# Kernel optimization log

Measured on AMD Instinct MI355X. Metric: run time of the kernel, lower is better.

The kernel has to match this reference:

```python
import jax, jax.numpy as jnp
import numpy as np

B, T, V, D, L, FFM = 2, 2048, 50257, 1024, 8, 2


def setup_inputs() -> dict:
    key = jax.random.key(0)
    ks = jax.random.split(key, 10)
    s = 0.02
    return {
        "input_ids": jax.random.randint(ks[0], (B, T), 0, V),
        "embed": jax.random.normal(ks[1], (V, D), jnp.float32) * s,
        "norm1_w": jnp.ones((L, D), jnp.float32),
        "norm2_w": jnp.ones((L, D), jnp.float32),
        "a_diag": jax.random.uniform(ks[2], (L, D), jnp.float32, 0.5, 0.99),
        "W_in": jax.random.normal(ks[3], (L, D, D), jnp.float32) * s,
        "b_in": jnp.zeros((L, D), jnp.float32),
        "W_out": jax.random.normal(ks[4], (L, D, D), jnp.float32) * s,
        "ff_w1": jax.random.normal(ks[5], (L, D, FFM * D), jnp.float32) * s,
        "ff_b1": jnp.zeros((L, FFM * D), jnp.float32),
        "ff_w2": jax.random.normal(ks[6], (L, FFM * D, D), jnp.float32) * s,
        "ff_b2": jnp.zeros((L, D), jnp.float32),
        "final_norm_w": jnp.ones((D,), jnp.float32),
        "lm_head_w": jax.random.normal(ks[7], (V, D), jnp.float32) * s,
    }


def rmsnorm(x, w, eps=1e-6):
    return x * jax.lax.rsqrt(jnp.mean(x * x, axis=-1, keepdims=True) + eps) * w


def chaos_core(x, a, Win, bin_, Wout):
    pre = jnp.einsum('btd,de->bte', x, Win) + bin_  # precompute input drive (parallel)

    def step(s, p):
        s = jnp.tanh(a * s + p)
        return s, s

    s0 = jnp.zeros((x.shape[0], x.shape[-1]), x.dtype)
    _, hs = jax.lax.scan(step, s0, jnp.swapaxes(pre, 0, 1))  # (T, B, D)
    hs = jnp.swapaxes(hs, 0, 1)  # (B, T, D)
    return jnp.einsum('btd,de->bte', hs, Wout)


def reference(input_ids, embed, norm1_w, norm2_w, a_diag, W_in, b_in, W_out,
              ff_w1, ff_b1, ff_w2, ff_b2, final_norm_w, lm_head_w):
    x = embed[input_ids]  # (B, T, D)
    for i in range(L):
        # input_norm -> core -> residual
        x = x + chaos_core(rmsnorm(x, norm1_w[i]), a_diag[i], W_in[i], b_in[i], W_out[i])
        # ff_norm -> FeedForward (Linear -> SiLU -> Linear) -> residual
        h = rmsnorm(x, norm2_w[i])
        h = jax.nn.silu(jnp.einsum('btd,df->btf', h, ff_w1[i]) + ff_b1[i])
        x = x + jnp.einsum('btf,fd->btd', h, ff_w2[i]) + ff_b2[i]
    x = rmsnorm(x, final_norm_w)
    return jnp.einsum('btd,vd->btv', x, lm_head_w)  # logits (B, T, V)
```

## Files before the change

### kernel.cpp

```cpp
#include <hip/hip_runtime.h>

typedef unsigned short u16;
typedef __bf16 bf16x8 __attribute__((ext_vector_type(8)));
typedef float f32x4 __attribute__((ext_vector_type(4)));
typedef unsigned short u16x4 __attribute__((ext_vector_type(4)));

__device__ __forceinline__ u16 f2bf(float f) {
  union { float f; unsigned int u; } v; v.f = f;
  return (u16)((v.u + 0x7FFFu + ((v.u >> 16) & 1u)) >> 16);
}

__device__ __forceinline__ void gload16(const void* g, void* l) {
  __builtin_amdgcn_global_load_lds(
      (const __attribute__((address_space(1))) unsigned int*)g,
      (__attribute__((address_space(3))) unsigned int*)l, 16, 0, 0);
}

__global__ void transpose_cast_kernel(const float* __restrict__ W, u16* __restrict__ WT,
                                      int R, int C) {
  __shared__ float tile[32][33];
  const int tx = threadIdx.x, ty = threadIdx.y;
  const size_t zoff = (size_t)blockIdx.z * R * C;
  const int c0 = blockIdx.x * 32, r0 = blockIdx.y * 32;
#pragma unroll
  for (int k = 0; k < 32; k += 8)
    tile[ty + k][tx] = W[zoff + (size_t)(r0 + ty + k) * C + (c0 + tx)];
  __syncthreads();
#pragma unroll
  for (int k = 0; k < 32; k += 8)
    WT[zoff + (size_t)(c0 + ty + k) * R + (r0 + tx)] = f2bf(tile[tx][ty + k]);
}

__global__ void lm_cast_kernel(const float* __restrict__ lm, u16* __restrict__ out) {
  const int row = blockIdx.x;
  const int t = threadIdx.x;
  u16x4 o = {0, 0, 0, 0};
  if (row < 50257) {
    float4 v = *(const float4*)(lm + (size_t)row * 1024 + t * 4);
    o.x = f2bf(v.x); o.y = f2bf(v.y); o.z = f2bf(v.z); o.w = f2bf(v.w);
  }
  *(u16x4*)(out + (size_t)row * 1024 + t * 4) = o;
}

__global__ void embed_kernel(const int* __restrict__ ids, const float* __restrict__ embed,
                             float* __restrict__ x) {
  const int row = blockIdx.x;
  const int id = ids[row];
  const int t = threadIdx.x;
  *(float4*)(x + (size_t)row * 1024 + t * 4) =
      *(const float4*)(embed + (size_t)id * 1024 + t * 4);
}

__global__ void rmsnorm_kernel(const float* __restrict__ x, const float* __restrict__ w,
                               u16* __restrict__ out) {
  const int row = blockIdx.x, tid = threadIdx.x;
  const float* xr = x + (size_t)row * 1024;
  float4 v = *(const float4*)(xr + tid * 4);
  float ss = v.x * v.x + v.y * v.y + v.z * v.z + v.w * v.w;
#pragma unroll
  for (int off = 32; off; off >>= 1) ss += __shfl_xor(ss, off);
  __shared__ float red[4];
  if ((tid & 63) == 0) red[tid >> 6] = ss;
  __syncthreads();
  const float tot = red[0] + red[1] + red[2] + red[3];
  const float r = rsqrtf(tot * (1.0f / 1024.0f) + 1e-6f);
  float4 wv = *(const float4*)(w + tid * 4);
  u16x4 o;
  o.x = f2bf(v.x * r * wv.x); o.y = f2bf(v.y * r * wv.y);
  o.z = f2bf(v.z * r * wv.z); o.w = f2bf(v.w * r * wv.w);
  *(u16x4*)(out + (size_t)row * 1024 + tid * 4) = o;
}

__device__ __forceinline__ void sload(const float* __restrict__ p, int tb,
                                      float A2b, float (&buf)[8]) {
#pragma unroll
  for (int j = 0; j < 8; j++)
    buf[j] = fmaf(p[(size_t)(tb + j) * 1024], 2.8853900817779268f, A2b);
}

__device__ __forceinline__ void scomp(float (&buf)[8], float m2A2, float& r,
                                      u16* __restrict__ o, int tb) {
#pragma unroll
  for (int j = 0; j < 8; j++) {
    float z = fmaf(m2A2, r, buf[j]);
    float e = __builtin_amdgcn_exp2f(z);
    r = __builtin_amdgcn_rcpf(1.0f + e);
    o[(size_t)(tb + j) * 1024] = f2bf(fmaf(-2.0f, r, 1.0f));
  }
}

__global__ __launch_bounds__(256) void scan_kernel(const float* __restrict__ pre,
                                                   const float* __restrict__ a_diag,
                                                   const float* __restrict__ b_in,
                                                   u16* __restrict__ hs) {
  const int T = 2048;
  const int idx = blockIdx.x * 256 + threadIdx.x;
  const int b = idx >> 10, d = idx & 1023;
  const float* p = pre + (size_t)b * T * 1024 + d;
  u16* o = hs + (size_t)b * T * 1024 + d;
  const float A2 = a_diag[d] * 2.8853900817779268f;
  const float A2b = fmaf(2.8853900817779268f, b_in[d], A2);
  const float m2A2 = -2.0f * A2;
  float r = 0.5f;
  float b0[8], b1[8], b2[8], b3[8];
  sload(p, 0, A2b, b0); sload(p, 8, A2b, b1);
  sload(p, 16, A2b, b2); sload(p, 24, A2b, b3);
  for (int t0 = 0; t0 < T; t0 += 32) {
    scomp(b0, m2A2, r, o, t0);
    if (t0 + 32 < T) sload(p, t0 + 32, A2b, b0);
    scomp(b1, m2A2, r, o, t0 + 8);
    if (t0 + 32 < T) sload(p, t0 + 40, A2b, b1);
    scomp(b2, m2A2, r, o, t0 + 16);
    if (t0 + 32 < T) sload(p, t0 + 48, A2b, b2);
    scomp(b3, m2A2, r, o, t0 + 24);
    if (t0 + 32 < T) sload(p, t0 + 56, A2b, b3);
  }
}

template <int EPI>
__global__ __launch_bounds__(256) void gemmL(
    const u16* __restrict__ A, int lda, const u16* __restrict__ Bw, int ldb,
    const float* __restrict__ bias, float* Cf, u16* __restrict__ Cb,
    int ldc, int K) {
  __shared__ char lds[49152];
  const int tid = threadIdx.x;
  const int lane = tid & 63;
  const int wc = tid >> 6;
  const int tm = blockIdx.y * 64, tn = blockIdx.x * 128;
  const int lr = lane & 15;
  const int sb0 = ((lane >> 4) ^ (lane & 7)) << 4;

  const int srow = tid >> 3;
  const int sxs = ((tid & 7) ^ (srow & 7)) << 4;
  const char* pA = (const char*)A + (size_t)(tm + srow) * lda * 2 + sxs;
  const char* pB = (const char*)Bw + (size_t)(tn + srow) * ldb * 2 + sxs;
  const size_t a32 = (size_t)lda * 64;
  const size_t b32 = (size_t)ldb * 64;

#define STGL(kt, bufo)                                \
  {                                                   \
    char* d = lds + (bufo) + tid * 16;                \
    const size_t kb = (size_t)(kt) << 7;              \
    gload16(pA + kb, d);                              \
    gload16(pA + a32 + kb, d + 4096);                 \
    gload16(pB + kb, d + 8192);                       \
    gload16(pB + b32 + kb, d + 12288);                \
    gload16(pB + 2 * b32 + kb, d + 16384);            \
    gload16(pB + 3 * b32 + kb, d + 20480);            \
  }

  f32x4 acc[4][2] = {};
  const int nkt = K >> 6;

  STGL(0, 0);
  int cur = 0;
  for (int kt = 0; kt < nkt; ++kt) {
    if (kt + 1 < nkt) {
      STGL(kt + 1, (cur ^ 1) * 24576);
      asm volatile("s_waitcnt vmcnt(6)" ::: "memory");
    } else {
      asm volatile("s_waitcnt vmcnt(0)" ::: "memory");
    }
    __builtin_amdgcn_s_barrier();
    const char* base = lds + cur * 24576;
    bf16x8 aF[4][2], bF[2][2];
#pragma unroll
    for (int m = 0; m < 4; m++)
#pragma unroll
      for (int ks = 0; ks < 2; ks++)
        aF[m][ks] =
            *(const bf16x8*)(base + (m * 16 + lr) * 128 + (sb0 ^ (ks << 6)));
#pragma unroll
    for (int n = 0; n < 2; n++)
#pragma unroll
      for (int ks = 0; ks < 2; ks++)
        bF[n][ks] = *(const bf16x8*)(base + 8192 +
                                     (wc * 32 + n * 16 + lr) * 128 +
                                     (sb0 ^ (ks << 6)));
#pragma unroll
    for (int ks = 0; ks < 2; ks++)
#pragma unroll
      for (int m = 0; m < 4; m++)
#pragma unroll
        for (int n = 0; n < 2; n++)
          acc[m][n] = __builtin_amdgcn_mfma_f32_16x16x32_bf16(
              aF[m][ks], bF[n][ks], acc[m][n], 0, 0, 0);
    __builtin_amdgcn_s_barrier();
    cur ^= 1;
  }
#undef STGL

  const int crow = tm + ((lane >> 4) << 2);
  const int ccol = tn + wc * 32 + lr;
#pragma unroll
  for (int m = 0; m < 4; m++) {
#pragma unroll
    for (int n = 0; n < 2; n++) {
      const int cg = ccol + n * 16;
      float bb = 0.0f;
      if (EPI == 2 || EPI == 3) bb = bias[cg];
#pragma unroll
      for (int j = 0; j < 4; j++) {
        const size_t off = (size_t)(crow + m * 16 + j) * ldc + cg;
        const float v = acc[m][n][j] + bb;
        if (EPI == 0) {
          Cf[off] = v;
        } else if (EPI == 1) {
          Cf[off] += v;
        } else if (EPI == 2) {
          const float sg = __builtin_amdgcn_rcpf(
              1.0f + __builtin_amdgcn_exp2f(-1.4426950408889634f * v));
          Cb[off] = f2bf(v * sg);
        } else {
          Cf[off] += v;
        }
      }
    }
  }
}

__global__ __launch_bounds__(512, 2) void gemm_lm8(
    const u16* __restrict__ A, const u16* __restrict__ Bw,
    float* __restrict__ C, int Nreal) {
  __shared__ char lds[131072];
  const int tid = threadIdx.x;
  const int lane = tid & 63;
  const int wid = tid >> 6;
  const int wr = wid >> 2;
  const int wc = wid & 3;
  const int bid = blockIdx.x;
  const int tm = (((bid & 7) << 1) + ((bid >> 3) & 1)) << 8;
  const int tn = (bid >> 4) << 8;

  const int srow = tid >> 3;
  const int sxor = ((tid & 7) ^ (srow & 7)) << 4;
  const char* pAs = (const char*)A + ((size_t)(tm + srow) << 11) + sxor;
  const char* pBs = (const char*)Bw + ((size_t)(tn + srow) << 11) + sxor;

#define STG(p, h, kt, ro)                                      \
  {                                                            \
    char* d = lds + (ro) + tid * 16;                           \
    const char* s = (p) + ((size_t)(h) << 18) + ((kt) << 7);   \
    gload16(s, d);                                             \
    gload16(s + (64ull << 11), d + 8192);                      \
  }

  const int lr = lane & 15;
  const int sb0 = (((lane >> 4) ^ (lane & 7)) << 4);
  const int sb[2] = {sb0, sb0 ^ 64};
  const int aB = wr * 16384 + lr * 128;
  const int bB = 32768 + (wc >> 1) * 16384 + ((wc & 1) * 64 + lr) * 128;

  bf16x8 aR[4][2], bR[2][2][2];
  f32x4 acc[8][4] = {};

#define LDA_Q(bufo, mq)                                                         \
  _Pragma("unroll") for (int m_ = 0; m_ < 4; m_++)                              \
  _Pragma("unroll") for (int k_ = 0; k_ < 2; k_++)                              \
      aR[m_][k_] = *(const bf16x8*)(lds + (bufo) + aB + (mq)*8192 + m_*2048 + sb[k_]);

#define LDB_Q(bufo, nq)                                                         \
  _Pragma("unroll") for (int n_ = 0; n_ < 2; n_++)                              \
  _Pragma("unroll") for (int k_ = 0; k_ < 2; k_++)                              \
      bR[nq][n_][k_] = *(const bf16x8*)(lds + (bufo) + bB + (nq)*4096 + n_*2048 + sb[k_]);

#define MFMA_Q(mq, nq)                                                          \
  __builtin_amdgcn_s_setprio(1);                                                \
  _Pragma("unroll") for (int m_ = 0; m_ < 4; m_++)                              \
  _Pragma("unroll") for (int n_ = 0; n_ < 2; n_++)                              \
  _Pragma("unroll") for (int k_ = 0; k_ < 2; k_++)                              \
      acc[(mq)*4 + m_][(nq)*2 + n_] = __builtin_amdgcn_mfma_f32_16x16x32_bf16(  \
          aR[m_][k_], bR[nq][n_][k_], acc[(mq)*4 + m_][(nq)*2 + n_], 0, 0, 0);  \
  __builtin_amdgcn_s_setprio(0);

#define BAR() __builtin_amdgcn_s_barrier()
#define LGKM0() asm volatile("s_waitcnt lgkmcnt(0)" ::: "memory")

  STG(pAs, 0, 0, 0);
  STG(pAs, 1, 0, 16384);
  STG(pBs, 0, 0, 32768);
  STG(pBs, 1, 0, 49152);
  STG(pBs, 0, 1, 65536 + 32768);
  STG(pBs, 1, 1, 65536 + 49152);
  asm volatile("s_waitcnt vmcnt(4)" ::: "memory");
  BAR();

  for (int it = 0; it < 8; ++it) {
    const int t1 = 2 * it + 1, t2 = 2 * it + 2, t3 = 2 * it + 3;
    const bool st = (it < 7);
    LDA_Q(0, 0); LDB_Q(0, 0);
    STG(pAs, 0, t1, 65536);
    BAR(); LGKM0(); MFMA_Q(0, 0); BAR();
    LDB_Q(0, 1);
    STG(pAs, 1, t1, 65536 + 16384);
    BAR(); LGKM0(); MFMA_Q(0, 1); BAR();
    LDA_Q(0, 1);
    if (st) STG(pBs, 0, t2, 32768);
    BAR(); LGKM0(); MFMA_Q(1, 0); BAR();
    if (st) STG(pBs, 1, t2, 49152);
    BAR(); LGKM0(); MFMA_Q(1, 1);
    if (st) { asm volatile("s_waitcnt vmcnt(4)" ::: "memory"); }
    else    { asm volatile("s_waitcnt vmcnt(0)" ::: "memory"); }
    BAR();
    LDA_Q(65536, 0); LDB_Q(65536, 0);
    if (st) STG(pAs, 0, t2, 0);
    BAR(); LGKM0(); MFMA_Q(0, 0); BAR();
    LDB_Q(65536, 1);
    if (st) STG(pAs, 1, t2, 16384);
    BAR(); LGKM0(); MFMA_Q(0, 1); BAR();
    LDA_Q(65536, 1);
    if (st) STG(pBs, 0, t3, 65536 + 32768);
    BAR(); LGKM0(); MFMA_Q(1, 0); BAR();
    if (st) STG(pBs, 1, t3, 65536 + 49152);
    BAR(); LGKM0(); MFMA_Q(1, 1);
    if (st) { asm volatile("s_waitcnt vmcnt(4)" ::: "memory"); }
    else    { asm volatile("s_waitcnt vmcnt(0)" ::: "memory"); }
    BAR();
  }
#undef STG
#undef LDA_Q
#undef LDB_Q
#undef MFMA_Q
#undef BAR
#undef LGKM0

  const int crow = tm + wr * 128 + ((lane >> 4) << 2);
  const int ccol = tn + wc * 64 + lr;
#pragma unroll
  for (int M_ = 0; M_ < 8; M_++) {
    const int r = crow + (M_ >> 2) * 64 + (M_ & 3) * 16;
#pragma unroll
    for (int N_ = 0; N_ < 4; N_++) {
      const int cg = ccol + (N_ >> 1) * 32 + (N_ & 1) * 16;
      if (cg < Nreal) {
#pragma unroll
        for (int j = 0; j < 4; j++)
          __builtin_nontemporal_store(acc[M_][N_][j],
                                      &C[(size_t)(r + j) * Nreal + cg]);
      }
    }
  }
}

extern "C" void kernel_launch(void* const* d_in, const int* in_sizes, int n_in,
                              void* d_out, int out_size, void* d_ws, size_t ws_size,
                              hipStream_t stream) {
  const int D = 1024, V = 50257, L = 8;
  const int M = 4096;
  const int Vpad = 50432;
  const size_t MD = (size_t)M * D;

  const int* ids = (const int*)d_in[0];
  const float* embedw = (const float*)d_in[1];
  const float* norm1_w = (const float*)d_in[2];
  const float* norm2_w = (const float*)d_in[3];
  const float* a_diag = (const float*)d_in[4];
  const float* W_in = (const float*)d_in[5];
  const float* b_in = (const float*)d_in[6];
  const float* W_out = (const float*)d_in[7];
  const float* ff_w1 = (const float*)d_in[8];
  const float* ff_b1 = (const float*)d_in[9];
  const float* ff_w2 = (const float*)d_in[10];
  const float* ff_b2 = (const float*)d_in[11];
  const float* final_norm_w = (const float*)d_in[12];
  const float* lm_head_w = (const float*)d_in[13];

  char* w = (char*)d_ws;
  float* x = (float*)w;   w += MD * 4;
  u16* h = (u16*)w;       w += MD * 2;
  float* pre = (float*)w; w += MD * 4;
  u16* hs = (u16*)w;      w += MD * 2;
  u16* hff = (u16*)w;     w += MD * 2 * 2;
  u16* WinT = (u16*)w;    w += (size_t)L * D * D * 2;
  u16* WoutT = (u16*)w;   w += (size_t)L * D * D * 2;
  u16* ffw1T = (u16*)w;   w += (size_t)L * 2 * D * D * 2;
  u16* ffw2T = (u16*)w;   w += (size_t)L * 2 * D * D * 2;
  u16* lmpad = (u16*)w;   w += (size_t)Vpad * D * 2;

  lm_cast_kernel<<<Vpad, 256, 0, stream>>>(lm_head_w, lmpad);
  transpose_cast_kernel<<<dim3(32, 32, L), dim3(32, 8), 0, stream>>>(W_in, WinT, D, D);
  transpose_cast_kernel<<<dim3(64, 32, L), dim3(32, 8), 0, stream>>>(ff_w1, ffw1T, D, 2 * D);
  transpose_cast_kernel<<<dim3(32, 32, L), dim3(32, 8), 0, stream>>>(W_out, WoutT, D, D);
  transpose_cast_kernel<<<dim3(32, 64, L), dim3(32, 8), 0, stream>>>(ff_w2, ffw2T, 2 * D, D);

  embed_kernel<<<M, 256, 0, stream>>>(ids, embedw, x);

  for (int l = 0; l < L; l++) {
    rmsnorm_kernel<<<M, 256, 0, stream>>>(x, norm1_w + (size_t)l * D, h);
    gemmL<0><<<dim3(8, 64), 256, 0, stream>>>(
        h, D, WinT + (size_t)l * D * D, D, nullptr, pre, nullptr, D, D);
    scan_kernel<<<8, 256, 0, stream>>>(pre, a_diag + (size_t)l * D,
                                       b_in + (size_t)l * D, hs);
    gemmL<1><<<dim3(8, 64), 256, 0, stream>>>(
        hs, D, WoutT + (size_t)l * D * D, D, nullptr, x, nullptr, D, D);
    rmsnorm_kernel<<<M, 256, 0, stream>>>(x, norm2_w + (size_t)l * D, h);
    gemmL<2><<<dim3(16, 64), 256, 0, stream>>>(
        h, D, ffw1T + (size_t)l * 2 * D * D, D, ff_b1 + (size_t)l * 2 * D,
        nullptr, hff, 2 * D, D);
    gemmL<3><<<dim3(8, 64), 256, 0, stream>>>(
        hff, 2 * D, ffw2T + (size_t)l * 2 * D * D, 2 * D,
        ff_b2 + (size_t)l * D, x, nullptr, D, 2 * D);
  }

  rmsnorm_kernel<<<M, 256, 0, stream>>>(x, final_norm_w, h);
  gemm_lm8<<<dim3(8 * 394), 512, 0, stream>>>(h, lmpad, (float*)d_out, V);
}
```

Measured before the change: 3.027 ms.

## Triple-buffer gemmL loads, fuse weight transpose kernels, drop nontemporal lm stores

The layer GEMM goes from double to triple buffering in LDS (72KB), prefetching two k-tiles ahead to hide more global-load latency. Its cost is lower occupancy from the larger LDS footprint. The four weight transpose/cast launches are merged into one flat-grid kernel to cut launch overhead. The LM-head output stores switch from nontemporal to regular stores.

```diff
diff --git a/kernel.cpp b/kernel.cpp
--- a/kernel.cpp
+++ b/kernel.cpp
@@ -16,19 +16,42 @@
       (__attribute__((address_space(3))) unsigned int*)l, 16, 0, 0);
 }
 
-__global__ void transpose_cast_kernel(const float* __restrict__ W, u16* __restrict__ WT,
-                                      int R, int C) {
+__global__ void prep_weights(const float* __restrict__ Win,
+                             const float* __restrict__ Wout,
+                             const float* __restrict__ ffw1,
+                             const float* __restrict__ ffw2,
+                             u16* __restrict__ WinT, u16* __restrict__ WoutT,
+                             u16* __restrict__ f1T, u16* __restrict__ f2T) {
   __shared__ float tile[32][33];
+  const int tk = blockIdx.x;
+  const float* src; u16* dst;
+  int R, C, tr, tc;
+  if (tk < 8192) {
+    const int l = tk >> 10, rem = tk & 1023;
+    R = 1024; C = 1024; tr = rem >> 5; tc = rem & 31;
+    src = Win + (size_t)l * 1048576; dst = WinT + (size_t)l * 1048576;
+  } else if (tk < 16384) {
+    const int q = tk - 8192, l = q >> 10, rem = q & 1023;
+    R = 1024; C = 1024; tr = rem >> 5; tc = rem & 31;
+    src = Wout + (size_t)l * 1048576; dst = WoutT + (size_t)l * 1048576;
+  } else if (tk < 32768) {
+    const int q = tk - 16384, l = q >> 11, rem = q & 2047;
+    R = 1024; C = 2048; tr = rem >> 6; tc = rem & 63;
+    src = ffw1 + (size_t)l * 2097152; dst = f1T + (size_t)l * 2097152;
+  } else {
+    const int q = tk - 32768, l = q >> 11, rem = q & 2047;
+    R = 2048; C = 1024; tr = rem >> 5; tc = rem & 31;
+    src = ffw2 + (size_t)l * 2097152; dst = f2T + (size_t)l * 2097152;
+  }
   const int tx = threadIdx.x, ty = threadIdx.y;
-  const size_t zoff = (size_t)blockIdx.z * R * C;
-  const int c0 = blockIdx.x * 32, r0 = blockIdx.y * 32;
+  const int c0 = tc * 32, r0 = tr * 32;
 #pragma unroll
   for (int k = 0; k < 32; k += 8)
-    tile[ty + k][tx] = W[zoff + (size_t)(r0 + ty + k) * C + (c0 + tx)];
+    tile[ty + k][tx] = src[(size_t)(r0 + ty + k) * C + (c0 + tx)];
   __syncthreads();
 #pragma unroll
   for (int k = 0; k < 32; k += 8)
-    WT[zoff + (size_t)(c0 + ty + k) * R + (r0 + tx)] = f2bf(tile[tx][ty + k]);
+    dst[(size_t)(c0 + ty + k) * R + (r0 + tx)] = f2bf(tile[tx][ty + k]);
 }
 
 __global__ void lm_cast_kernel(const float* __restrict__ lm, u16* __restrict__ out) {
@@ -122,7 +145,7 @@
     const u16* __restrict__ A, int lda, const u16* __restrict__ Bw, int ldb,
     const float* __restrict__ bias, float* Cf, u16* __restrict__ Cb,
     int ldc, int K) {
-  __shared__ char lds[49152];
+  __shared__ char lds[73728];
   const int tid = threadIdx.x;
   const int lane = tid & 63;
   const int wc = tid >> 6;
@@ -153,16 +176,20 @@
   const int nkt = K >> 6;
 
   STGL(0, 0);
-  int cur = 0;
+  STGL(1, 24576);
+  int cb = 0;
   for (int kt = 0; kt < nkt; ++kt) {
-    if (kt + 1 < nkt) {
-      STGL(kt + 1, (cur ^ 1) * 24576);
+    if (kt + 2 < nkt) {
+      const int nb = cb + 49152 >= 73728 ? cb - 24576 : cb + 49152;
+      STGL(kt + 2, nb);
+      asm volatile("s_waitcnt vmcnt(12)" ::: "memory");
+    } else if (kt + 1 < nkt) {
       asm volatile("s_waitcnt vmcnt(6)" ::: "memory");
     } else {
       asm volatile("s_waitcnt vmcnt(0)" ::: "memory");
     }
     __builtin_amdgcn_s_barrier();
-    const char* base = lds + cur * 24576;
+    const char* base = lds + cb;
     bf16x8 aF[4][2], bF[2][2];
 #pragma unroll
     for (int m = 0; m < 4; m++)
@@ -186,7 +213,7 @@
           acc[m][n] = __builtin_amdgcn_mfma_f32_16x16x32_bf16(
               aF[m][ks], bF[n][ks], acc[m][n], 0, 0, 0);
     __builtin_amdgcn_s_barrier();
-    cur ^= 1;
+    cb = (cb + 24576 == 73728) ? 0 : cb + 24576;
   }
 #undef STGL
 
@@ -335,8 +362,7 @@
       if (cg < Nreal) {
 #pragma unroll
         for (int j = 0; j < 4; j++)
-          __builtin_nontemporal_store(acc[M_][N_][j],
-                                      &C[(size_t)(r + j) * Nreal + cg]);
+          C[(size_t)(r + j) * Nreal + cg] = acc[M_][N_][j];
       }
     }
   }
@@ -377,12 +403,9 @@
   u16* ffw2T = (u16*)w;   w += (size_t)L * 2 * D * D * 2;
   u16* lmpad = (u16*)w;   w += (size_t)Vpad * D * 2;
 
+  prep_weights<<<49152, dim3(32, 8), 0, stream>>>(
+      W_in, W_out, ff_w1, ff_w2, WinT, WoutT, ffw1T, ffw2T);
   lm_cast_kernel<<<Vpad, 256, 0, stream>>>(lm_head_w, lmpad);
-  transpose_cast_kernel<<<dim3(32, 32, L), dim3(32, 8), 0, stream>>>(W_in, WinT, D, D);
-  transpose_cast_kernel<<<dim3(64, 32, L), dim3(32, 8), 0, stream>>>(ff_w1, ffw1T, D, 2 * D);
-  transpose_cast_kernel<<<dim3(32, 32, L), dim3(32, 8), 0, stream>>>(W_out, WoutT, D, D);
-  transpose_cast_kernel<<<dim3(32, 64, L), dim3(32, 8), 0, stream>>>(ff_w2, ffw2T, 2 * D, D);
-
   embed_kernel<<<M, 256, 0, stream>>>(ids, embedw, x);
 
   for (int l = 0; l < L; l++) {
```

Result: faster. 2.712 ms (-10.4%).
